# Kernel tuning notes

Measured on AMD Instinct MI355X. Metric: run time of the kernel, lower is better.

## Reference

```python
import jax, jax.numpy as jnp
import numpy as np

D_MODEL = 1024
NUM_HEADS = 16
D_K = D_MODEL // NUM_HEADS


def setup_inputs() -> dict:
    key = jax.random.key(0)
    ks = jax.random.split(key, 11)
    B, S = 2, 2048
    scale = 1.0 / np.sqrt(D_MODEL)
    inp = {
        "q": jax.random.normal(ks[0], (B, S, D_MODEL), jnp.float32),
        "k": jax.random.normal(ks[1], (B, S, D_MODEL), jnp.float32),
        "v": jax.random.normal(ks[2], (B, S, D_MODEL), jnp.float32),
        "Wq": jax.random.normal(ks[3], (D_MODEL, D_MODEL), jnp.float32) * scale,
        "bq": jnp.zeros((D_MODEL,), jnp.float32),
        "Wk": jax.random.normal(ks[4], (D_MODEL, D_MODEL), jnp.float32) * scale,
        "bk": jnp.zeros((D_MODEL,), jnp.float32),
        "Wv": jax.random.normal(ks[5], (D_MODEL, D_MODEL), jnp.float32) * scale,
        "bv": jnp.zeros((D_MODEL,), jnp.float32),
        "Wo": jax.random.normal(ks[6], (D_MODEL, D_MODEL), jnp.float32) * scale,
        "bo": jnp.zeros((D_MODEL,), jnp.float32),
    }
    return inp


def _split_heads(x):
    B, S, _ = x.shape
    return x.reshape(B, S, NUM_HEADS, D_K).transpose(0, 2, 1, 3)  # [B,H,S,dk]


def reference(q, k, v, Wq, bq, Wk, bk, Wv, bv, Wo, bo):
    Q = _split_heads(q @ Wq.T + bq)  # [B,H,S,dk]
    K = _split_heads(k @ Wk.T + bk)
    V = _split_heads(v @ Wv.T + bv)
    scores = jnp.einsum("bhqd,bhkd->bhqk", Q, K) / jnp.sqrt(jnp.float32(D_K))
    attn = jax.nn.softmax(scores, axis=-1)
    ctx = jnp.einsum("bhqk,bhkd->bhqd", attn, V)  # [B,H,S,dk]
    B, H, S, dk = ctx.shape
    ctx = ctx.transpose(0, 2, 1, 3).reshape(B, S, D_MODEL)
    return ctx @ Wo.T + bo
```

## Files before the change

kernel.cpp:

```cpp
#include <hip/hip_runtime.h>
#include <hip/hip_bf16.h>

typedef unsigned short ushort_t;
typedef __attribute__((ext_vector_type(4))) float f32x4;
typedef __attribute__((ext_vector_type(16))) float f32x16;
typedef __attribute__((ext_vector_type(8))) short short8;
typedef __attribute__((ext_vector_type(4))) unsigned short us4;

#define D_MODEL 1024
#define NHEAD 16
#define DK 64
#define BATCH 2
#define SEQ 2048
#define MTOT 4096
#define EX (MTOT * D_MODEL)
#define EW (D_MODEL * D_MODEL)

#define MFMA16(a,b,c) __builtin_amdgcn_mfma_f32_16x16x32_bf16((a),(b),(c),0,0,0)
#define MFMA32(a,b,c) __builtin_amdgcn_mfma_f32_32x32x16_bf16((a),(b),(c),0,0,0)

__device__ __forceinline__ ushort_t f2bf(float f){
    union{float f;unsigned u;}c; c.f=f;
    unsigned u=c.u, r=u+0x7FFFu+((u>>16)&1u);
    return (ushort_t)(r>>16);
}
__device__ __forceinline__ unsigned cvtpk_bf(float a, float b){
    float2 t; t.x = a; t.y = b;
    union{ __hip_bfloat162 h; unsigned u; } c;
    c.h = __float22bfloat162_rn(t);
    return c.u;
}
__device__ __forceinline__ void plswap(unsigned &a, unsigned &b){
    asm volatile("v_permlane32_swap_b32 %0, %1" : "+v"(a), "+v"(b));
}
__device__ __forceinline__ void gload16(const ushort_t* g, ushort_t* l){
    __builtin_amdgcn_global_load_lds((const __attribute__((address_space(1))) unsigned*)g,
                                     (__attribute__((address_space(3))) unsigned*)l, 16, 0, 0);
}
__device__ __forceinline__ int xcd_swz(int nwg){
    int s = blockIdx.x;
    return (s & 7) * (nwg >> 3) + (s >> 3);
}

__global__ void cast1(const float* __restrict__ x, ushort_t* __restrict__ y, int n4){
    int i = blockIdx.x*blockDim.x + threadIdx.x, st = gridDim.x*blockDim.x;
    for(; i < n4; i += st){
        f32x4 v = ((const f32x4*)x)[i];
        us4 o; o[0]=f2bf(v[0]); o[1]=f2bf(v[1]); o[2]=f2bf(v[2]); o[3]=f2bf(v[3]);
        ((us4*)y)[i] = o;
    }
}
__global__ void cast4(const float* __restrict__ a, const float* __restrict__ b,
                      const float* __restrict__ c, const float* __restrict__ d4,
                      ushort_t* __restrict__ dst, int n4){
    const float* s = blockIdx.y==0 ? a : (blockIdx.y==1 ? b : (blockIdx.y==2 ? c : d4));
    us4* d = (us4*)(dst + (size_t)blockIdx.y * n4 * 4);
    const f32x4* sv = (const f32x4*)s;
    int i = blockIdx.x*blockDim.x + threadIdx.x, st = gridDim.x*blockDim.x;
    for(; i < n4; i += st){
        f32x4 v = sv[i];
        us4 o; o[0]=f2bf(v[0]); o[1]=f2bf(v[1]); o[2]=f2bf(v[2]); o[3]=f2bf(v[3]);
        d[i] = o;
    }
}

__device__ __forceinline__ void gemm_body(
    const ushort_t* __restrict__ A, const ushort_t* __restrict__ Bm,
    const float* __restrict__ bias, float scale, int bm, int bn, int mode,
    void* __restrict__ out,
    ushort_t* As0, ushort_t* As1, ushort_t* Bs0, ushort_t* Bs1)
{
    const int tid = threadIdx.x, lane = tid & 63, wid = tid >> 6;
    const int row0 = bm << 7, col0 = bn << 7;
    const int wrow = (wid >> 1) << 6, wcol = (wid & 1) << 6;
    const int l4 = lane >> 2, lc = (lane & 3) << 3, lr = lane & 15, ko = (lane >> 4) << 3;
    const f32x4 Z4 = {0.f,0.f,0.f,0.f};

    f32x4 acc[4][4];
#pragma unroll
    for(int i=0;i<4;i++)
#pragma unroll
        for(int j=0;j<4;j++) acc[i][j] = Z4;

#define GSTAGE(AS,BS,k0) do{ \
    gload16(A +(size_t)(row0+32*wid   +l4)*D_MODEL+(k0)+lc, (AS)+(2*wid  )*512); \
    gload16(A +(size_t)(row0+32*wid+16+l4)*D_MODEL+(k0)+lc, (AS)+(2*wid+1)*512); \
    gload16(Bm+(size_t)(col0+32*wid   +l4)*D_MODEL+(k0)+lc, (BS)+(2*wid  )*512); \
    gload16(Bm+(size_t)(col0+32*wid+16+l4)*D_MODEL+(k0)+lc, (BS)+(2*wid+1)*512); \
}while(0)
#define GCOMP(AS,BS) do{ \
    short8 af[4], bf[4]; \
    _Pragma("unroll") for(int i=0;i<4;i++) af[i]=*(const short8*)((AS)+(wrow+i*16+lr)*32+ko); \
    _Pragma("unroll") for(int j=0;j<4;j++) bf[j]=*(const short8*)((BS)+(wcol+j*16+lr)*32+ko); \
    __builtin_amdgcn_s_setprio(1); \
    _Pragma("unroll") for(int i=0;i<4;i++) \
    _Pragma("unroll") for(int j=0;j<4;j++) acc[i][j]=MFMA16(af[i],bf[j],acc[i][j]); \
    __builtin_amdgcn_s_setprio(0); \
}while(0)

    GSTAGE(As0,Bs0,0);
    __syncthreads();
#pragma unroll 1
    for(int t=0; t<32; t+=2){
        if(t+1<32) GSTAGE(As1,Bs1,(t+1)*32);
        GCOMP(As0,Bs0);
        __syncthreads();
        if(t+2<32) GSTAGE(As0,Bs0,(t+2)*32);
        GCOMP(As1,Bs1);
        __syncthreads();
    }
#undef GSTAGE

    const int rr4 = (lane >> 4) << 2;
#pragma unroll
    for(int i=0;i<4;i++){
#pragma unroll
        for(int j=0;j<4;j++){
            const int m0 = row0 + wrow + i*16 + rr4;
            const int n  = col0 + wcol + j*16 + lr;
            const float bs = bias[n];
            if(mode == 2){
                float* O = (float*)out;
#pragma unroll
                for(int r=0;r<4;r++) O[(size_t)(m0+r)*D_MODEL+n] = (acc[i][j][r]+bs)*scale;
            } else if(mode == 0){
                ushort_t* O = (ushort_t*)out;
#pragma unroll
                for(int r=0;r<4;r++) O[(size_t)(m0+r)*D_MODEL+n] = f2bf((acc[i][j][r]+bs)*scale);
            } else {
                ushort_t* O = (ushort_t*)out;
                const int bb = m0 >> 11, s = m0 & 2047, h = n >> 6, d = n & 63;
                us4 p;
#pragma unroll
                for(int r=0;r<4;r++) p[r] = f2bf((acc[i][j][r]+bs)*scale);
                *(us4*)(O + ((size_t)(bb*NHEAD + h)*DK + d)*SEQ + s) = p;
            }
        }
    }
#undef GCOMP
}

#define QSCALE (0.125f * 1.44269504088896f)

__global__ __launch_bounds__(256,2)
void qkv_fused(const float* __restrict__ Xq, const float* __restrict__ Xk,
               const float* __restrict__ Xv,
               const ushort_t* __restrict__ Wq, const ushort_t* __restrict__ Wk,
               const ushort_t* __restrict__ Wv,
               const float* __restrict__ bq, const float* __restrict__ bk,
               const float* __restrict__ bv,
               ushort_t* Qp, ushort_t* Kp, ushort_t* VtG)
{
    __shared__ ushort_t As0[4096], As1[4096], Bs0[4096], Bs1[4096];
    const int wk = xcd_swz(768);
    const int which = wk >> 8, t = wk & 255;
    const float *Af; const ushort_t *Bm; const float* bias; float scale; int mode; void* out;
    if(which == 0){ Af=Xq; Bm=Wq; bias=bq; scale=QSCALE; mode=0; out=Qp; }
    else if(which == 1){ Af=Xk; Bm=Wk; bias=bk; scale=1.f; mode=0; out=Kp; }
    else { Af=Xv; Bm=Wv; bias=bv; scale=1.f; mode=1; out=VtG; }

    const int bm = t >> 3, bn = t & 7;
    const int tid = threadIdx.x, lane = tid & 63, wid = tid >> 6;
    const int row0 = bm << 7, col0 = bn << 7;
    const int wrow = (wid >> 1) << 6, wcol = (wid & 1) << 6;
    const int l4 = lane >> 2, lc = (lane & 3) << 3, lr = lane & 15, ko = (lane >> 4) << 3;
    const f32x4 Z4 = {0.f,0.f,0.f,0.f};

    f32x4 acc[4][4];
#pragma unroll
    for(int i=0;i<4;i++)
#pragma unroll
        for(int j=0;j<4;j++) acc[i][j] = Z4;

    f32x4 ar[2][2][2];

#define ALOAD(R, k0) do{ \
    _Pragma("unroll") for(int c=0;c<2;c++){ \
        const float* src = Af + (size_t)(row0+32*wid+16*c+l4)*D_MODEL + (k0)+lc; \
        (R)[c][0] = *(const f32x4*)(src); \
        (R)[c][1] = *(const f32x4*)(src+4); \
    } \
}while(0)
#define AWRITE(AS, R) do{ \
    _Pragma("unroll") for(int c=0;c<2;c++){ \
        union{ unsigned u[4]; short8 s; } P; \
        P.u[0]=cvtpk_bf((R)[c][0][0],(R)[c][0][1]); \
        P.u[1]=cvtpk_bf((R)[c][0][2],(R)[c][0][3]); \
        P.u[2]=cvtpk_bf((R)[c][1][0],(R)[c][1][1]); \
        P.u[3]=cvtpk_bf((R)[c][1][2],(R)[c][1][3]); \
        *(short8*)((AS) + (2*wid+c)*512 + lane*8) = P.s; \
    } \
}while(0)
#define BSTAGE(BS,k0) do{ \
    gload16(Bm+(size_t)(col0+32*wid   +l4)*D_MODEL+(k0)+lc, (BS)+(2*wid  )*512); \
    gload16(Bm+(size_t)(col0+32*wid+16+l4)*D_MODEL+(k0)+lc, (BS)+(2*wid+1)*512); \
}while(0)
#define GCOMP(AS,BS) do{ \
    short8 af[4], bf[4]; \
    _Pragma("unroll") for(int i=0;i<4;i++) af[i]=*(const short8*)((AS)+(wrow+i*16+lr)*32+ko); \
    _Pragma("unroll") for(int j=0;j<4;j++) bf[j]=*(const short8*)((BS)+(wcol+j*16+lr)*32+ko); \
    __builtin_amdgcn_s_setprio(1); \
    _Pragma("unroll") for(int i=0;i<4;i++) \
    _Pragma("unroll") for(int j=0;j<4;j++) acc[i][j]=MFMA16(af[i],bf[j],acc[i][j]); \
    __builtin_amdgcn_s_setprio(0); \
}while(0)

    ALOAD(ar[0], 0); BSTAGE(Bs0, 0);
    AWRITE(As0, ar[0]);
    __syncthreads();
#pragma unroll 1
    for(int t2=0; t2<32; t2+=2){
        if(t2+1<32){ ALOAD(ar[1], (t2+1)*32); BSTAGE(Bs1, (t2+1)*32); }
        GCOMP(As0,Bs0);
        if(t2+1<32) AWRITE(As1, ar[1]);
        __syncthreads();
        if(t2+2<32){ ALOAD(ar[0], (t2+2)*32); BSTAGE(Bs0, (t2+2)*32); }
        GCOMP(As1,Bs1);
        if(t2+2<32) AWRITE(As0, ar[0]);
        __syncthreads();
    }
#undef ALOAD
#undef AWRITE
#undef BSTAGE
#undef GCOMP

    const int rr4 = (lane >> 4) << 2;
#pragma unroll
    for(int i=0;i<4;i++){
#pragma unroll
        for(int j=0;j<4;j++){
            const int m0 = row0 + wrow + i*16 + rr4;
            const int n  = col0 + wcol + j*16 + lr;
            const float bs = bias[n];
            if(mode == 0){
                ushort_t* O = (ushort_t*)out;
#pragma unroll
                for(int r=0;r<4;r++) O[(size_t)(m0+r)*D_MODEL+n] = f2bf((acc[i][j][r]+bs)*scale);
            } else {
                ushort_t* O = (ushort_t*)out;
                const int bb = m0 >> 11, s = m0 & 2047, h = n >> 6, d = n & 63;
                us4 p;
#pragma unroll
                for(int r=0;r<4;r++) p[r] = f2bf((acc[i][j][r]+bs)*scale);
                *(us4*)(O + ((size_t)(bb*NHEAD + h)*DK + d)*SEQ + s) = p;
            }
        }
    }
}

__global__ __launch_bounds__(256,2)
void gemm_out_bf(const ushort_t* __restrict__ A, const ushort_t* __restrict__ Bm,
                 const float* __restrict__ bias, float* __restrict__ out)
{
    __shared__ ushort_t As0[4096], As1[4096];
    __shared__ ushort_t Bs0[2048], Bs1[2048];
    const int wk = xcd_swz(512);
    const int bm = wk >> 4, bn = wk & 15;
    const int tid = threadIdx.x, lane = tid & 63, wid = tid >> 6;
    const int row0 = bm << 7, col0 = bn << 6;
    const int wrow = (wid >> 1) << 6, wcol = (wid & 1) << 5;
    const int l4 = lane >> 2, lc = (lane & 3) << 3, lr = lane & 15, ko = (lane >> 4) << 3;
    const f32x4 Z4 = {0.f,0.f,0.f,0.f};

    f32x4 acc[4][2];
#pragma unroll
    for(int i=0;i<4;i++){ acc[i][0] = Z4; acc[i][1] = Z4; }

#define OSTAGE(AS,BS,k0) do{ \
    gload16(A +(size_t)(row0+32*wid   +l4)*D_MODEL+(k0)+lc, (AS)+(2*wid  )*512); \
    gload16(A +(size_t)(row0+32*wid+16+l4)*D_MODEL+(k0)+lc, (AS)+(2*wid+1)*512); \
    gload16(Bm+(size_t)(col0+16*wid+l4)*D_MODEL+(k0)+lc,    (BS)+wid*512); \
}while(0)
#define OCOMP(AS,BS) do{ \
    short8 af[4], bf2[2]; \
    _Pragma("unroll") for(int i=0;i<4;i++) af[i]=*(const short8*)((AS)+(wrow+i*16+lr)*32+ko); \
    _Pragma("unroll") for(int j=0;j<2;j++) bf2[j]=*(const short8*)((BS)+(wcol+j*16+lr)*32+ko); \
    __builtin_amdgcn_s_setprio(1); \
    _Pragma("unroll") for(int i=0;i<4;i++) \
    _Pragma("unroll") for(int j=0;j<2;j++) acc[i][j]=MFMA16(af[i],bf2[j],acc[i][j]); \
    __builtin_amdgcn_s_setprio(0); \
}while(0)

    OSTAGE(As0,Bs0,0);
    __syncthreads();
#pragma unroll 1
    for(int t=0; t<32; t+=2){
        if(t+1<32) OSTAGE(As1,Bs1,(t+1)*32);
        OCOMP(As0,Bs0);
        __syncthreads();
        if(t+2<32) OSTAGE(As0,Bs0,(t+2)*32);
        OCOMP(As1,Bs1);
        __syncthreads();
    }
#undef OSTAGE
#undef OCOMP

    const int rr4 = (lane >> 4) << 2;
#pragma unroll
    for(int i=0;i<4;i++)
#pragma unroll
        for(int j=0;j<2;j++){
            const int m0 = row0 + wrow + i*16 + rr4;
            const int n  = col0 + wcol + j*16 + lr;
            const float bs = bias[n];
#pragma unroll
            for(int r=0;r<4;r++) out[(size_t)(m0+r)*D_MODEL+n] = acc[i][j][r] + bs;
        }
}

__global__ __launch_bounds__(256,2)
void gemm_one(const ushort_t* __restrict__ A, const ushort_t* __restrict__ Bm,
              const float* __restrict__ bias, float scale, int mode, void* out)
{
    __shared__ ushort_t As0[4096], As1[4096], Bs0[4096], Bs1[4096];
    const int wk = xcd_swz(256);
    gemm_body(A,Bm,bias,scale, wk>>3, wk&7, mode, out, As0,As1,Bs0,Bs1);
}

__global__ __launch_bounds__(256,4)
void attn_half(const ushort_t* __restrict__ Qp, const ushort_t* __restrict__ Kp,
               const ushort_t* __restrict__ VtG, ushort_t* __restrict__ ctx)
{
    __shared__ ushort_t KV[4][64*64];

    const int wk = xcd_swz(1024);
    const int bh = wk >> 5, qt = wk & 31;
    const int b = bh >> 4, h = bh & 15;
    const int tid = threadIdx.x, lane = tid & 63, wid = tid >> 6;
    const int qgrp = wid & 1, half = wid >> 1;
    const int lq = lane & 31, hi = lane >> 5, lx = lq & 7;
    const size_t qkbase = (size_t)b*SEQ*D_MODEL + h*DK;
    const size_t vbase  = (size_t)bh * DK * SEQ;
    const int q0 = qt*64 + qgrp*32;
    const int kvbase = half * (SEQ/2);

    ushort_t* Ksb = KV[half*2];
    ushort_t* Vsb = KV[half*2+1];

    short8 qa[4];
#pragma unroll
    for(int s=0;s<4;s++)
        qa[s] = *(const short8*)(Qp + qkbase + (size_t)(q0+lq)*D_MODEL + s*16 + hi*8);

    const f32x16 Z16 = {0.f,0.f,0.f,0.f,0.f,0.f,0.f,0.f,0.f,0.f,0.f,0.f,0.f,0.f,0.f,0.f};
    f32x16 o[2];
    float2 run_l2; run_l2.x = 0.f; run_l2.y = 0.f;
    o[0] = Z16; o[1] = Z16;

    const int srow = lane >> 3;
    const int jsw  = (((lane & 7) ^ srow) << 3);

#pragma unroll 1
    for(int kv0 = 0; kv0 < SEQ/2; kv0 += 64){
#pragma unroll
        for(int c=0;c<4;c++){
            const int rb = qgrp*32 + c*8;
            gload16(Kp  + qkbase + (size_t)(kvbase+kv0+rb+srow)*D_MODEL + jsw, Ksb + rb*64);
            gload16(VtG + vbase  + (size_t)(rb+srow)*SEQ + kvbase+kv0 + jsw,   Vsb + rb*64);
        }
        __syncthreads();

        f32x16 st0, st1;
        __builtin_amdgcn_s_setprio(1);
        {
            f32x16 acc = Z16;
#pragma unroll
            for(int s=0;s<4;s++){
                short8 kf = *(const short8*)(Ksb + lq*64 + (((2*s+hi)^lx)<<3));
                acc = MFMA32(kf, qa[s], acc);
            }
            st0 = acc;
        }
        {
            f32x16 acc = Z16;
#pragma unroll
            for(int s=0;s<4;s++){
                short8 kf = *(const short8*)(Ksb + (32+lq)*64 + (((2*s+hi)^lx)<<3));
                acc = MFMA32(kf, qa[s], acc);
            }
            st1 = acc;
        }
        __builtin_amdgcn_s_setprio(0);

#pragma unroll
        for(int i=0;i<16;i++){
            st0[i] = exp2f(st0[i]);
            st1[i] = exp2f(st1[i]);
        }
        float2 t2[8];
#pragma unroll
        for(int i=0;i<8;i++){
            t2[i].x = st0[2*i] + st1[2*i];
            t2[i].y = st0[2*i+1] + st1[2*i+1];
        }
#pragma unroll
        for(int w=4;w;w>>=1)
#pragma unroll
            for(int i=0;i<w;i++){ t2[i].x += t2[i+w].x; t2[i].y += t2[i+w].y; }
        run_l2.x += t2[0].x; run_l2.y += t2[0].y;

#pragma unroll
        for(int sub=0; sub<2; sub++){
            unsigned w8[8];
#pragma unroll
            for(int i=0;i<8;i++)
                w8[i] = cvtpk_bf(sub==0 ? st0[2*i] : st1[2*i], sub==0 ? st0[2*i+1] : st1[2*i+1]);
            plswap(w8[0], w8[2]); plswap(w8[1], w8[3]);
            plswap(w8[4], w8[6]); plswap(w8[5], w8[7]);
            union { unsigned u[4]; short8 s; } p0, p1;
            p0.u[0]=w8[0]; p0.u[1]=w8[1]; p0.u[2]=w8[2]; p0.u[3]=w8[3];
            p1.u[0]=w8[4]; p1.u[1]=w8[5]; p1.u[2]=w8[6]; p1.u[3]=w8[7];
            __builtin_amdgcn_s_setprio(1);
#pragma unroll
            for(int ds=0; ds<2; ds++){
                short8 v0 = *(const short8*)(Vsb + (ds*32+lq)*64 + (((sub*4+0+hi)^lx)<<3));
                short8 v1 = *(const short8*)(Vsb + (ds*32+lq)*64 + (((sub*4+2+hi)^lx)<<3));
                o[ds] = MFMA32(v0, p0.s, o[ds]);
                o[ds] = MFMA32(v1, p1.s, o[ds]);
            }
            __builtin_amdgcn_s_setprio(0);
        }
        __syncthreads();
    }

    float lsum = run_l2.x + run_l2.y;
    lsum += __shfl_xor(lsum, 32);

    float* Xo = (float*)&KV[0][0];
    float* Xl = Xo + 64*68;
    if(half == 1){
#pragma unroll
        for(int ds=0; ds<2; ds++)
#pragma unroll
            for(int g=0; g<4; g++){
                f32x4 v; v[0]=o[ds][4*g+0]; v[1]=o[ds][4*g+1]; v[2]=o[ds][4*g+2]; v[3]=o[ds][4*g+3];
                *(f32x4*)(Xo + (qgrp*32+lq)*68 + ds*32 + 8*g + 4*hi) = v;
            }
        if(hi == 0) Xl[qgrp*32+lq] = lsum;
    }
    __syncthreads();
    if(half == 0){
        const float inv = 1.f / (lsum + Xl[qgrp*32+lq]);
#pragma unroll
        for(int ds=0; ds<2; ds++)
#pragma unroll
            for(int g=0; g<4; g++){
                f32x4 oo = *(const f32x4*)(Xo + (qgrp*32+lq)*68 + ds*32 + 8*g + 4*hi);
                unsigned lo  = cvtpk_bf((o[ds][4*g+0]+oo[0])*inv, (o[ds][4*g+1]+oo[1])*inv);
                unsigned hi2 = cvtpk_bf((o[ds][4*g+2]+oo[2])*inv, (o[ds][4*g+3]+oo[3])*inv);
                union { unsigned u[2]; us4 v; } pp; pp.u[0]=lo; pp.u[1]=hi2;
                *(us4*)(ctx + qkbase + (size_t)(q0+lq)*D_MODEL + ds*32 + 8*g + 4*hi) = pp.v;
            }
    }
}

__global__ __launch_bounds__(128,2)
void attn_fwd(const ushort_t* __restrict__ Qp, const ushort_t* __restrict__ Kp,
              const ushort_t* __restrict__ VtG, ushort_t* __restrict__ ctx)
{
    __shared__ ushort_t Ks0[64*64], Ks1[64*64];
    __shared__ ushort_t Vs0[64*64], Vs1[64*64];

    const int wk = xcd_swz(1024);
    const int bh = wk >> 5, qt = wk & 31;
    const int b = bh >> 4, h = bh & 15;
    const int tid = threadIdx.x, lane = tid & 63, wid = tid >> 6;
    const int lq = lane & 31, hi = lane >> 5, lx = lq & 7;
    const size_t qkbase = (size_t)b*SEQ*D_MODEL + h*DK;
    const size_t vbase  = (size_t)bh * DK * SEQ;
    const int q0 = qt*64 + wid*32;

    short8 qa[4];
#pragma unroll
    for(int s=0;s<4;s++)
        qa[s] = *(const short8*)(Qp + qkbase + (size_t)(q0+lq)*D_MODEL + s*16 + hi*8);

    f32x16 o[2];
    float run_m = -1e30f, run_l = 0.f;
#pragma unroll
    for(int i=0;i<16;i++){ o[0][i] = 0.f; o[1][i] = 0.f; }

    const int srow = lane >> 3;
    const int jsw  = (((lane & 7) ^ srow) << 3);

#define ASTAGE(KS, VS, kv) do{ \
    _Pragma("unroll") for(int c=0;c<4;c++){ \
        const int rb = wid*32 + c*8; \
        gload16(Kp  + qkbase + (size_t)((kv)+rb+srow)*D_MODEL + jsw, (KS) + rb*64); \
        gload16(VtG + vbase  + (size_t)(rb+srow)*SEQ + (kv) + jsw,   (VS) + rb*64); \
    } \
}while(0)

#define APHASE(KS, VS) do{ \
    f32x16 st0, st1; \
    __builtin_amdgcn_s_setprio(1); \
    { f32x16 acc; \
      _Pragma("unroll") for(int i=0;i<16;i++) acc[i]=0.f; \
      _Pragma("unroll") for(int s=0;s<4;s++){ \
          short8 kf = *(const short8*)((KS) + lq*64 + (((2*s+hi)^lx)<<3)); \
          acc = MFMA32(kf, qa[s], acc); } \
      st0 = acc; } \
    { f32x16 acc; \
      _Pragma("unroll") for(int i=0;i<16;i++) acc[i]=0.f; \
      _Pragma("unroll") for(int s=0;s<4;s++){ \
          short8 kf = *(const short8*)((KS) + (32+lq)*64 + (((2*s+hi)^lx)<<3)); \
          acc = MFMA32(kf, qa[s], acc); } \
      st1 = acc; } \
    __builtin_amdgcn_s_setprio(0); \
    float tr[8]; \
    _Pragma("unroll") for(int i=0;i<8;i++) tr[i] = fmaxf(fmaxf(st0[i],st0[i+8]), fmaxf(st1[i],st1[i+8])); \
    _Pragma("unroll") for(int w=4;w;w>>=1) \
    _Pragma("unroll") for(int i=0;i<w;i++) tr[i]=fmaxf(tr[i],tr[i+w]); \
    const float pmax = fmaxf(tr[0], __shfl_xor(tr[0], 32)); \
    if(__any(pmax > run_m + 8.f)){ \
        const float nm = fmaxf(run_m, pmax); \
        const float corr = exp2f(run_m - nm); \
        run_m = nm; run_l *= corr; \
        _Pragma("unroll") for(int i=0;i<16;i++){ o[0][i]*=corr; o[1][i]*=corr; } \
    } \
    float ts[16]; \
    _Pragma("unroll") for(int i=0;i<16;i++){ \
        st0[i] = exp2f(st0[i] - run_m); \
        st1[i] = exp2f(st1[i] - run_m); \
        ts[i] = st0[i] + st1[i]; } \
    _Pragma("unroll") for(int w=8;w;w>>=1) \
    _Pragma("unroll") for(int i=0;i<w;i++) ts[i]+=ts[i+w]; \
    run_l += ts[0] + __shfl_xor(ts[0], 32); \
    _Pragma("unroll") for(int sub=0; sub<2; sub++){ \
        unsigned w8[8]; \
        _Pragma("unroll") for(int i=0;i<8;i++) \
            w8[i] = cvtpk_bf(sub==0 ? st0[2*i] : st1[2*i], sub==0 ? st0[2*i+1] : st1[2*i+1]); \
        plswap(w8[0], w8[2]); plswap(w8[1], w8[3]); \
        plswap(w8[4], w8[6]); plswap(w8[5], w8[7]); \
        union { unsigned u[4]; short8 s; } p0, p1; \
        p0.u[0]=w8[0]; p0.u[1]=w8[1]; p0.u[2]=w8[2]; p0.u[3]=w8[3]; \
        p1.u[0]=w8[4]; p1.u[1]=w8[5]; p1.u[2]=w8[6]; p1.u[3]=w8[7]; \
        __builtin_amdgcn_s_setprio(1); \
        _Pragma("unroll") for(int ds=0; ds<2; ds++){ \
            short8 v0 = *(const short8*)((VS) + (ds*32+lq)*64 + (((sub*4+0+hi)^lx)<<3)); \
            short8 v1 = *(const short8*)((VS) + (ds*32+lq)*64 + (((sub*4+2+hi)^lx)<<3)); \
            o[ds] = MFMA32(v0, p0.s, o[ds]); \
            o[ds] = MFMA32(v1, p1.s, o[ds]); } \
        __builtin_amdgcn_s_setprio(0); \
    } \
}while(0)

    ASTAGE(Ks0, Vs0, 0);
    __syncthreads();
#pragma unroll 1
    for(int kv0 = 0; kv0 < SEQ; kv0 += 128){
        if(kv0 + 64 < SEQ) ASTAGE(Ks1, Vs1, kv0 + 64);
        APHASE(Ks0, Vs0);
        __syncthreads();
        if(kv0 + 128 < SEQ) ASTAGE(Ks0, Vs0, kv0 + 128);
        APHASE(Ks1, Vs1);
        __syncthreads();
    }
#undef ASTAGE

    const float linv = 1.f / run_l;
#pragma unroll
    for(int ds=0; ds<2; ds++)
#pragma unroll
        for(int g=0; g<4; g++){
            unsigned lo = cvtpk_bf(o[ds][4*g+0]*linv, o[ds][4*g+1]*linv);
            unsigned hi2 = cvtpk_bf(o[ds][4*g+2]*linv, o[ds][4*g+3]*linv);
            union { unsigned u[2]; us4 v; } pp; pp.u[0]=lo; pp.u[1]=hi2;
            *(us4*)(ctx + qkbase + (size_t)(q0+lq)*D_MODEL + ds*32 + 8*g + 4*hi) = pp.v;
        }
}

extern "C" void kernel_launch(void* const* d_in, const int* in_sizes, int n_in,
                              void* d_out, int out_size, void* d_ws, size_t ws_size,
                              hipStream_t stream) {
    (void)in_sizes; (void)n_in; (void)out_size;
    const float* q  = (const float*)d_in[0];
    const float* k  = (const float*)d_in[1];
    const float* v  = (const float*)d_in[2];
    const float* Wq = (const float*)d_in[3];
    const float* bq = (const float*)d_in[4];
    const float* Wk = (const float*)d_in[5];
    const float* bk = (const float*)d_in[6];
    const float* Wv = (const float*)d_in[7];
    const float* bv = (const float*)d_in[8];
    const float* Wo = (const float*)d_in[9];
    const float* bo = (const float*)d_in[10];
    float* out = (float*)d_out;

    ushort_t* WS = (ushort_t*)d_ws;
    const dim3 blk(256);
    const int n4x = EX/4, n4w = EW/4;

    const size_t tierA = ((size_t)4*EW + (size_t)4*EX) * 2;

    if(ws_size >= tierA){
        ushort_t* Wqb = WS;
        ushort_t* Wkb = Wqb + EW;
        ushort_t* Wvb = Wkb + EW;
        ushort_t* Wob = Wvb + EW;
        ushort_t* Qp  = Wob + EW;
        ushort_t* Kp  = Qp + EX;
        ushort_t* VtG = Kp + EX;
        ushort_t* ctx = VtG + EX;

        cast4<<<dim3(256,4), blk, 0, stream>>>(Wq, Wk, Wv, Wo, Wqb, n4w);
        qkv_fused<<<768, blk, 0, stream>>>(q, k, v, Wqb, Wkb, Wvb, bq, bk, bv, Qp, Kp, VtG);
        attn_half<<<1024, blk, 0, stream>>>(Qp, Kp, VtG, ctx);
        gemm_out_bf<<<512, blk, 0, stream>>>(ctx, Wob, bo, out);
    } else {
        ushort_t* Xb  = WS;
        ushort_t* Wb  = Xb + EX;
        ushort_t* Qp  = Wb + EW;
        ushort_t* Kp  = Qp + EX;
        ushort_t* VtG = Kp + EX;
        ushort_t* ctx = Xb;

        cast1<<<1024, blk, 0, stream>>>(q, Xb, n4x);
        cast1<<<512,  blk, 0, stream>>>(Wq, Wb, n4w);
        gemm_one<<<256, blk, 0, stream>>>(Xb, Wb, bq, QSCALE, 0, Qp);
        cast1<<<1024, blk, 0, stream>>>(k, Xb, n4x);
        cast1<<<512,  blk, 0, stream>>>(Wk, Wb, n4w);
        gemm_one<<<256, blk, 0, stream>>>(Xb, Wb, bk, 1.f, 0, Kp);
        cast1<<<1024, blk, 0, stream>>>(v, Xb, n4x);
        cast1<<<512,  blk, 0, stream>>>(Wv, Wb, n4w);
        gemm_one<<<256, blk, 0, stream>>>(Xb, Wb, bv, 1.f, 1, VtG);
        attn_fwd<<<1024, dim3(128), 0, stream>>>(Qp, Kp, VtG, ctx);
        cast1<<<512, blk, 0, stream>>>(Wo, Wb, n4w);
        gemm_one<<<256, blk, 0, stream>>>(ctx, Wb, bo, 1.f, 2, out);
    }
}
```

Measured before the change: 127.2 us.

## Prefetch next K/V tile into registers and use padded LDS rows in attn_half

Replaces the direct global-to-LDS loads in the split-KV attention kernel with register prefetch of the next K/V tile, issued before the current tile's MFMA work. The tile is written to LDS after a barrier. The XOR-swizzled LDS layout becomes a padded row stride of 68 elements. The aim is to hide global load latency behind the QK and PV compute. The cost is 8 extra short8 registers per thread, an extra barrier per iteration, and LDS traffic through VGPRs, which may reduce occupancy at 4 blocks per CU.

```diff
diff --git a/kernel.cpp b/kernel.cpp
--- a/kernel.cpp
+++ b/kernel.cpp
@@ -15,6 +15,7 @@
 #define MTOT 4096
 #define EX (MTOT * D_MODEL)
 #define EW (D_MODEL * D_MODEL)
+#define RS 68
 
 #define MFMA16(a,b,c) __builtin_amdgcn_mfma_f32_16x16x32_bf16((a),(b),(c),0,0,0)
 #define MFMA32(a,b,c) __builtin_amdgcn_mfma_f32_32x32x16_bf16((a),(b),(c),0,0,0)
@@ -321,14 +322,14 @@
 void attn_half(const ushort_t* __restrict__ Qp, const ushort_t* __restrict__ Kp,
                const ushort_t* __restrict__ VtG, ushort_t* __restrict__ ctx)
 {
-    __shared__ ushort_t KV[4][64*64];
+    __shared__ ushort_t KV[4][64*RS];
 
     const int wk = xcd_swz(1024);
     const int bh = wk >> 5, qt = wk & 31;
     const int b = bh >> 4, h = bh & 15;
     const int tid = threadIdx.x, lane = tid & 63, wid = tid >> 6;
     const int qgrp = wid & 1, half = wid >> 1;
-    const int lq = lane & 31, hi = lane >> 5, lx = lq & 7;
+    const int lq = lane & 31, hi = lane >> 5;
     const size_t qkbase = (size_t)b*SEQ*D_MODEL + h*DK;
     const size_t vbase  = (size_t)bh * DK * SEQ;
     const int q0 = qt*64 + qgrp*32;
@@ -337,6 +338,9 @@
     ushort_t* Ksb = KV[half*2];
     ushort_t* Vsb = KV[half*2+1];
 
+    const int srow = lane >> 3;
+    const int scol = (lane & 7) << 3;
+
     short8 qa[4];
 #pragma unroll
     for(int s=0;s<4;s++)
@@ -347,18 +351,31 @@
     float2 run_l2; run_l2.x = 0.f; run_l2.y = 0.f;
     o[0] = Z16; o[1] = Z16;
 
-    const int srow = lane >> 3;
-    const int jsw  = (((lane & 7) ^ srow) << 3);
+    short8 kr[4], vr[4];
+
+#define PLOAD(kv) do{ \
+    _Pragma("unroll") for(int c=0;c<4;c++){ \
+        const int r_ = qgrp*32 + c*8 + srow; \
+        kr[c] = *(const short8*)(Kp  + qkbase + (size_t)(kvbase+(kv)+r_)*D_MODEL + scol); \
+        vr[c] = *(const short8*)(VtG + vbase  + (size_t)r_*SEQ + kvbase+(kv) + scol); \
+    } \
+}while(0)
+#define PWRITE() do{ \
+    _Pragma("unroll") for(int c=0;c<4;c++){ \
+        const int r_ = qgrp*32 + c*8 + srow; \
+        *(short8*)(Ksb + r_*RS + scol) = kr[c]; \
+        *(short8*)(Vsb + r_*RS + scol) = vr[c]; \
+    } \
+}while(0)
+
+    PLOAD(0);
+    PWRITE();
+    __syncthreads();
 
 #pragma unroll 1
     for(int kv0 = 0; kv0 < SEQ/2; kv0 += 64){
-#pragma unroll
-        for(int c=0;c<4;c++){
-            const int rb = qgrp*32 + c*8;
-            gload16(Kp  + qkbase + (size_t)(kvbase+kv0+rb+srow)*D_MODEL + jsw, Ksb + rb*64);
-            gload16(VtG + vbase  + (size_t)(rb+srow)*SEQ + kvbase+kv0 + jsw,   Vsb + rb*64);
-        }
-        __syncthreads();
+        const bool more = (kv0 + 64 < SEQ/2);
+        if(more) PLOAD(kv0 + 64);
 
         f32x16 st0, st1;
         __builtin_amdgcn_s_setprio(1);
@@ -366,7 +383,7 @@
             f32x16 acc = Z16;
 #pragma unroll
             for(int s=0;s<4;s++){
-                short8 kf = *(const short8*)(Ksb + lq*64 + (((2*s+hi)^lx)<<3));
+                short8 kf = *(const short8*)(Ksb + lq*RS + (2*s+hi)*8);
                 acc = MFMA32(kf, qa[s], acc);
             }
             st0 = acc;
@@ -375,7 +392,7 @@
             f32x16 acc = Z16;
 #pragma unroll
             for(int s=0;s<4;s++){
-                short8 kf = *(const short8*)(Ksb + (32+lq)*64 + (((2*s+hi)^lx)<<3));
+                short8 kf = *(const short8*)(Ksb + (32+lq)*RS + (2*s+hi)*8);
                 acc = MFMA32(kf, qa[s], acc);
             }
             st1 = acc;
@@ -413,28 +430,35 @@
             __builtin_amdgcn_s_setprio(1);
 #pragma unroll
             for(int ds=0; ds<2; ds++){
-                short8 v0 = *(const short8*)(Vsb + (ds*32+lq)*64 + (((sub*4+0+hi)^lx)<<3));
-                short8 v1 = *(const short8*)(Vsb + (ds*32+lq)*64 + (((sub*4+2+hi)^lx)<<3));
+                short8 v0 = *(const short8*)(Vsb + (ds*32+lq)*RS + (sub*4+0+hi)*8);
+                short8 v1 = *(const short8*)(Vsb + (ds*32+lq)*RS + (sub*4+2+hi)*8);
                 o[ds] = MFMA32(v0, p0.s, o[ds]);
                 o[ds] = MFMA32(v1, p1.s, o[ds]);
             }
             __builtin_amdgcn_s_setprio(0);
         }
-        __syncthreads();
-    }
+
+        __syncthreads();
+        if(more){
+            PWRITE();
+            __syncthreads();
+        }
+    }
+#undef PLOAD
+#undef PWRITE
 
     float lsum = run_l2.x + run_l2.y;
     lsum += __shfl_xor(lsum, 32);
 
     float* Xo = (float*)&KV[0][0];
-    float* Xl = Xo + 64*68;
+    float* Xl = Xo + 64*RS;
     if(half == 1){
 #pragma unroll
         for(int ds=0; ds<2; ds++)
 #pragma unroll
             for(int g=0; g<4; g++){
                 f32x4 v; v[0]=o[ds][4*g+0]; v[1]=o[ds][4*g+1]; v[2]=o[ds][4*g+2]; v[3]=o[ds][4*g+3];
-                *(f32x4*)(Xo + (qgrp*32+lq)*68 + ds*32 + 8*g + 4*hi) = v;
+                *(f32x4*)(Xo + (qgrp*32+lq)*RS + ds*32 + 8*g + 4*hi) = v;
             }
         if(hi == 0) Xl[qgrp*32+lq] = lsum;
     }
@@ -445,7 +469,7 @@
         for(int ds=0; ds<2; ds++)
 #pragma unroll
             for(int g=0; g<4; g++){
-                f32x4 oo = *(const f32x4*)(Xo + (qgrp*32+lq)*68 + ds*32 + 8*g + 4*hi);
+                f32x4 oo = *(const f32x4*)(Xo + (qgrp*32+lq)*RS + ds*32 + 8*g + 4*hi);
                 unsigned lo  = cvtpk_bf((o[ds][4*g+0]+oo[0])*inv, (o[ds][4*g+1]+oo[1])*inv);
                 unsigned hi2 = cvtpk_bf((o[ds][4*g+2]+oo[2])*inv, (o[ds][4*g+3]+oo[3])*inv);
                 union { unsigned u[2]; us4 v; } pp; pp.u[0]=lo; pp.u[1]=hi2;
```

Result: slower. 246.9 us (+94.2%).

## Prefetch K/V tiles through registers with padded LDS rows and smaller KV steps

Applied to the files above, without the earlier changes.

Replaces the direct global-to-LDS swizzled loads in the attention kernel with a register prefetch of the next K/V tile, issued before the current tile's MFMAs and written to LDS afterwards. The LDS tiles now use padded row strides instead of an XOR swizzle. The KV step shrinks from 64 to 32 keys, so each iteration does a single score MFMA block and half the PV work. The goal is to hide global load latency behind compute, at the cost of twice as many iterations, extra barriers per iteration and more register pressure.

```diff
diff --git a/kernel.cpp b/kernel.cpp
--- a/kernel.cpp
+++ b/kernel.cpp
@@ -15,6 +15,8 @@
 #define MTOT 4096
 #define EX (MTOT * D_MODEL)
 #define EW (D_MODEL * D_MODEL)
+#define RSK 68
+#define RSV 36
 
 #define MFMA16(a,b,c) __builtin_amdgcn_mfma_f32_16x16x32_bf16((a),(b),(c),0,0,0)
 #define MFMA32(a,b,c) __builtin_amdgcn_mfma_f32_32x32x16_bf16((a),(b),(c),0,0,0)
@@ -321,21 +323,24 @@
 void attn_half(const ushort_t* __restrict__ Qp, const ushort_t* __restrict__ Kp,
                const ushort_t* __restrict__ VtG, ushort_t* __restrict__ ctx)
 {
-    __shared__ ushort_t KV[4][64*64];
+    __shared__ ushort_t SMEM[2 * (32*RSK + 64*RSV)];
 
     const int wk = xcd_swz(1024);
     const int bh = wk >> 5, qt = wk & 31;
     const int b = bh >> 4, h = bh & 15;
     const int tid = threadIdx.x, lane = tid & 63, wid = tid >> 6;
     const int qgrp = wid & 1, half = wid >> 1;
-    const int lq = lane & 31, hi = lane >> 5, lx = lq & 7;
+    const int lq = lane & 31, hi = lane >> 5;
     const size_t qkbase = (size_t)b*SEQ*D_MODEL + h*DK;
     const size_t vbase  = (size_t)bh * DK * SEQ;
     const int q0 = qt*64 + qgrp*32;
     const int kvbase = half * (SEQ/2);
 
-    ushort_t* Ksb = KV[half*2];
-    ushort_t* Vsb = KV[half*2+1];
+    ushort_t* Ksb = SMEM + half * (32*RSK + 64*RSV);
+    ushort_t* Vsb = Ksb + 32*RSK;
+
+    const int krow = lane >> 3, kcol = (lane & 7) << 3;
+    const int vrow = lane >> 2, vcol = (lane & 3) << 3;
 
     short8 qa[4];
 #pragma unroll
@@ -344,67 +349,63 @@
 
     const f32x16 Z16 = {0.f,0.f,0.f,0.f,0.f,0.f,0.f,0.f,0.f,0.f,0.f,0.f,0.f,0.f,0.f,0.f};
     f32x16 o[2];
-    float2 run_l2; run_l2.x = 0.f; run_l2.y = 0.f;
+    float run_l = 0.f;
     o[0] = Z16; o[1] = Z16;
 
-    const int srow = lane >> 3;
-    const int jsw  = (((lane & 7) ^ srow) << 3);
+    short8 kr0, kr1, vr0, vr1;
+
+#define PLOAD(kv) do{ \
+    kr0 = *(const short8*)(Kp  + qkbase + (size_t)(kvbase+(kv)+qgrp*16         +krow)*D_MODEL + kcol); \
+    kr1 = *(const short8*)(Kp  + qkbase + (size_t)(kvbase+(kv)+qgrp*16 + 8     +krow)*D_MODEL + kcol); \
+    vr0 = *(const short8*)(VtG + vbase  + (size_t)(qgrp*32      + vrow)*SEQ + kvbase+(kv) + vcol); \
+    vr1 = *(const short8*)(VtG + vbase  + (size_t)(qgrp*32 + 16 + vrow)*SEQ + kvbase+(kv) + vcol); \
+}while(0)
+#define PWRITE() do{ \
+    *(short8*)(Ksb + (qgrp*16     + krow)*RSK + kcol) = kr0; \
+    *(short8*)(Ksb + (qgrp*16 + 8 + krow)*RSK + kcol) = kr1; \
+    *(short8*)(Vsb + (qgrp*32      + vrow)*RSV + vcol) = vr0; \
+    *(short8*)(Vsb + (qgrp*32 + 16 + vrow)*RSV + vcol) = vr1; \
+}while(0)
+
+    PLOAD(0);
+    PWRITE();
+    __syncthreads();
 
 #pragma unroll 1
-    for(int kv0 = 0; kv0 < SEQ/2; kv0 += 64){
-#pragma unroll
-        for(int c=0;c<4;c++){
-            const int rb = qgrp*32 + c*8;
-            gload16(Kp  + qkbase + (size_t)(kvbase+kv0+rb+srow)*D_MODEL + jsw, Ksb + rb*64);
-            gload16(VtG + vbase  + (size_t)(rb+srow)*SEQ + kvbase+kv0 + jsw,   Vsb + rb*64);
-        }
-        __syncthreads();
-
-        f32x16 st0, st1;
+    for(int kv0 = 0; kv0 < SEQ/2; kv0 += 32){
+        const bool more = (kv0 + 32 < SEQ/2);
+        if(more) PLOAD(kv0 + 32);
+
+        f32x16 st;
         __builtin_amdgcn_s_setprio(1);
         {
             f32x16 acc = Z16;
 #pragma unroll
             for(int s=0;s<4;s++){
-                short8 kf = *(const short8*)(Ksb + lq*64 + (((2*s+hi)^lx)<<3));
+                short8 kf = *(const short8*)(Ksb + lq*RSK + (2*s+hi)*8);
                 acc = MFMA32(kf, qa[s], acc);
             }
-            st0 = acc;
-        }
+            st = acc;
+        }
+        __builtin_amdgcn_s_setprio(0);
+
+#pragma unroll
+        for(int i=0;i<16;i++) st[i] = exp2f(st[i]);
         {
-            f32x16 acc = Z16;
-#pragma unroll
-            for(int s=0;s<4;s++){
-                short8 kf = *(const short8*)(Ksb + (32+lq)*64 + (((2*s+hi)^lx)<<3));
-                acc = MFMA32(kf, qa[s], acc);
-            }
-            st1 = acc;
-        }
-        __builtin_amdgcn_s_setprio(0);
-
-#pragma unroll
-        for(int i=0;i<16;i++){
-            st0[i] = exp2f(st0[i]);
-            st1[i] = exp2f(st1[i]);
-        }
-        float2 t2[8];
-#pragma unroll
-        for(int i=0;i<8;i++){
-            t2[i].x = st0[2*i] + st1[2*i];
-            t2[i].y = st0[2*i+1] + st1[2*i+1];
-        }
-#pragma unroll
-        for(int w=4;w;w>>=1)
-#pragma unroll
-            for(int i=0;i<w;i++){ t2[i].x += t2[i+w].x; t2[i].y += t2[i+w].y; }
-        run_l2.x += t2[0].x; run_l2.y += t2[0].y;
-
-#pragma unroll
-        for(int sub=0; sub<2; sub++){
+            float s8[8];
+#pragma unroll
+            for(int i=0;i<8;i++) s8[i] = st[i] + st[i+8];
+#pragma unroll
+            for(int w=4;w;w>>=1)
+#pragma unroll
+                for(int i=0;i<w;i++) s8[i] += s8[i+w];
+            run_l += s8[0];
+        }
+
+        {
             unsigned w8[8];
 #pragma unroll
-            for(int i=0;i<8;i++)
-                w8[i] = cvtpk_bf(sub==0 ? st0[2*i] : st1[2*i], sub==0 ? st0[2*i+1] : st1[2*i+1]);
+            for(int i=0;i<8;i++) w8[i] = cvtpk_bf(st[2*i], st[2*i+1]);
             plswap(w8[0], w8[2]); plswap(w8[1], w8[3]);
             plswap(w8[4], w8[6]); plswap(w8[5], w8[7]);
             union { unsigned u[4]; short8 s; } p0, p1;
@@ -413,20 +414,27 @@
             __builtin_amdgcn_s_setprio(1);
 #pragma unroll
             for(int ds=0; ds<2; ds++){
-                short8 v0 = *(const short8*)(Vsb + (ds*32+lq)*64 + (((sub*4+0+hi)^lx)<<3));
-                short8 v1 = *(const short8*)(Vsb + (ds*32+lq)*64 + (((sub*4+2+hi)^lx)<<3));
+                short8 v0 = *(const short8*)(Vsb + (ds*32+lq)*RSV + (0+hi)*8);
+                short8 v1 = *(const short8*)(Vsb + (ds*32+lq)*RSV + (2+hi)*8);
                 o[ds] = MFMA32(v0, p0.s, o[ds]);
                 o[ds] = MFMA32(v1, p1.s, o[ds]);
             }
             __builtin_amdgcn_s_setprio(0);
         }
-        __syncthreads();
-    }
-
-    float lsum = run_l2.x + run_l2.y;
+
+        __syncthreads();
+        if(more){
+            PWRITE();
+            __syncthreads();
+        }
+    }
+#undef PLOAD
+#undef PWRITE
+
+    float lsum = run_l;
     lsum += __shfl_xor(lsum, 32);
 
-    float* Xo = (float*)&KV[0][0];
+    float* Xo = (float*)&SMEM[0];
     float* Xl = Xo + 64*68;
     if(half == 1){
 #pragma unroll
```

Measured after the change: 227.9 us. +79.2%, slower.
